# Kernel optimization log

Hardware: AMD Instinct MI355X
Metric: run time of the kernel (lower is better)

The kernel has to match this reference:

```python
import jax, jax.numpy as jnp
import numpy as np

_PRIME = 31
SIZES = tuple(range(3, 21))          # 18 n-gram sizes
TBL = 4096                            # hash table size
MIXED = TBL                           # dedicated mixed/special bucket id
NUM_SIZES_P1 = len(SIZES) + 1         # normalizer (19)
B, L, D = 8, 8192, 256


def _ngram_ids(byte_ids):
    """Rolling polynomial hash ids for every n in SIZES.

    Incremental recurrence: h_k[i] = (h_{k-1}[i-1] * 31 + safe[i]) % TBL
    gives the hash of the backward k-gram ending at i, computing each prefix
    once instead of from scratch per size (same math as the torch loops).
    Returns list of [B, L] int32 id arrays, one per size in SIZES.
    """
    dna_map = jnp.full((14,), -1, dtype=jnp.int32)
    dna_map = dna_map.at[jnp.array([1, 2, 3, 4])].set(jnp.array([0, 1, 2, 3], dtype=jnp.int32))
    dna_idx = dna_map[byte_ids]                      # [B, L], -1 for non-DNA
    safe = jnp.maximum(dna_idx, 0)
    bad1 = dna_idx == -1

    h = safe          # window size k=1 hash
    bad = bad1        # any special token in window / incomplete window
    ids = []
    for k in range(2, max(SIZES) + 1):
        # shift previous-position state right by 1; pad start as bad (incomplete window)
        h = (jnp.pad(h[:, :-1], ((0, 0), (1, 0))) * _PRIME + safe) % TBL
        bad = jnp.pad(bad[:, :-1], ((0, 0), (1, 0)), constant_values=True) | bad1
        if k in SIZES:
            ids.append(jnp.where(bad, MIXED, h))
    return ids


def setup_inputs() -> dict:
    key = jax.random.key(0)
    k1, k2 = jax.random.split(key)
    byte_ids = jax.random.randint(k1, (B, L), 0, 14, dtype=jnp.int32)
    # 18 embedding tables, each [TBL+1, D] (last row = mixed bucket)
    tables = jax.random.normal(k2, (len(SIZES), TBL + 1, D), dtype=jnp.float32) * 0.02
    return {"byte_ids": byte_ids, "tables": tables}


def reference(byte_ids, tables):
    ids = _ngram_ids(byte_ids)
    total = jnp.zeros(byte_ids.shape + (tables.shape[-1],), dtype=tables.dtype)
    for t, id_n in enumerate(ids):
        total = total + tables[t][id_n]            # [B, L, D] gather-accumulate
    return total / NUM_SIZES_P1
```

## Files before the change

### kernel.cpp

```cpp
#include <hip/hip_runtime.h>

#define TBLSZ 4096
#define NSIZES 18
#define DIM 256
#define SEQLEN 8192

__global__ void NGram_smix_kernel(const float* __restrict__ tables,
                                  float* __restrict__ smix) {
    int d = threadIdx.x;
    float s = 0.f;
    for (int t = 0; t < NSIZES; ++t)
        s += tables[((size_t)t * (TBLSZ + 1) + TBLSZ) * DIM + d];
    smix[d] = s;
}

__global__ __launch_bounds__(256) void NGramEmbedding_73718818668652_kernel(
    const int* __restrict__ byte_ids, const float* __restrict__ tables,
    const float* __restrict__ smix, float* __restrict__ out, int npos)
{
    const int tid0   = blockIdx.x * blockDim.x + threadIdx.x;
    const int stride = gridDim.x * blockDim.x;
    const int c = tid0 & 63;
    const float4 base = ((const float4*)smix)[c];
    const float inv = 1.0f / 19.0f;
    const int total = npos * 64;

    for (int tid = tid0; tid < total; tid += stride) {
        const int pos = tid >> 6;
        const int i   = pos & (SEQLEN - 1);
        const int* row = byte_ids + (pos - i);

        float4 acc = base;

        bool slow = false;
        if (i >= 2) {
            int v0 = row[i], v1 = row[i - 1], v2 = row[i - 2];
            slow = ((unsigned)(v0 - 1) < 4u) & ((unsigned)(v1 - 1) < 4u)
                 & ((unsigned)(v2 - 1) < 4u);
        }

        if (slow) {
            int h = 0, p = 1;
            for (int j = 0; j < 20; ++j) {
                const int q = i - j;
                const int v = (q >= 0) ? row[q] : 0;
                if ((unsigned)(v - 1) >= 4u) break;
                h = (h + (v - 1) * p) & (TBLSZ - 1);
                p = (p * 31) & (TBLSZ - 1);
                const int k = j + 1;
                if (k >= 3) {
                    const int t = k - 3;
                    const float4* T4 =
                        (const float4*)(tables + (size_t)t * (TBLSZ + 1) * DIM);
                    float4 g = T4[(size_t)h * (DIM / 4) + c];
                    float4 m = T4[(size_t)TBLSZ * (DIM / 4) + c];
                    acc.x += g.x - m.x; acc.y += g.y - m.y;
                    acc.z += g.z - m.z; acc.w += g.w - m.w;
                }
            }
        }

        float4 r;
        r.x = acc.x * inv; r.y = acc.y * inv;
        r.z = acc.z * inv; r.w = acc.w * inv;
        ((float4*)out)[(size_t)pos * (DIM / 4) + c] = r;
    }
}

extern "C" void kernel_launch(void* const* d_in, const int* in_sizes, int n_in,
                              void* d_out, int out_size, void* d_ws, size_t ws_size,
                              hipStream_t stream) {
    const int*   byte_ids = (const int*)d_in[0];
    const float* tables   = (const float*)d_in[1];
    float* out  = (float*)d_out;
    float* smix = (float*)d_ws;
    const int npos = in_sizes[0];

    hipLaunchKernelGGL(NGram_smix_kernel, dim3(1), dim3(256), 0, stream,
                       tables, smix);
    hipLaunchKernelGGL(NGramEmbedding_73718818668652_kernel,
                       dim3(4096), dim3(256), 0, stream,
                       byte_ids, tables, smix, out, npos);
}
```

Baseline: 24.49 us.

## Split into broadcast fill kernel and sparse ballot-driven correction kernel

The single pass is replaced by a dedicated fill kernel that writes the scaled mixed-bucket sum to every output row, plus a correction kernel. In the correction kernel each lane checks one position and uses a wave ballot to loop only over positions whose last three tokens are DNA, overwriting those rows. The intent is to keep the bulk store loop free of per-position branch checks and to do the hash lookups only where needed. The cost is an extra launch and a second write to the corrected rows.

```diff
diff --git a/kernel.cpp b/kernel.cpp
--- a/kernel.cpp
+++ b/kernel.cpp
@@ -4,66 +4,81 @@
 #define NSIZES 18
 #define DIM 256
 #define SEQLEN 8192
+#define INV19 (1.0f / 19.0f)
 
-__global__ void NGram_smix_kernel(const float* __restrict__ tables,
-                                  float* __restrict__ smix) {
+__global__ void k_smix(const float* __restrict__ tables, float* __restrict__ smix) {
     int d = threadIdx.x;
     float s = 0.f;
+#pragma unroll
     for (int t = 0; t < NSIZES; ++t)
         s += tables[((size_t)t * (TBLSZ + 1) + TBLSZ) * DIM + d];
-    smix[d] = s;
+    smix[d] = s * INV19;
 }
 
-__global__ __launch_bounds__(256) void NGramEmbedding_73718818668652_kernel(
+__global__ __launch_bounds__(256) void k_fill(const float* __restrict__ smix,
+                                              float4* __restrict__ out, int total_f4) {
+    const int t = blockIdx.x * 256 + threadIdx.x;
+    const int stride = gridDim.x * 256;
+    const float4 v = ((const float4*)smix)[t & 63];
+#pragma unroll 4
+    for (int f = t; f < total_f4; f += stride)
+        out[f] = v;
+}
+
+__global__ __launch_bounds__(256) void k_correct(
     const int* __restrict__ byte_ids, const float* __restrict__ tables,
     const float* __restrict__ smix, float* __restrict__ out, int npos)
 {
-    const int tid0   = blockIdx.x * blockDim.x + threadIdx.x;
-    const int stride = gridDim.x * blockDim.x;
-    const int c = tid0 & 63;
-    const float4 base = ((const float4*)smix)[c];
-    const float inv = 1.0f / 19.0f;
-    const int total = npos * 64;
+    const int lane = threadIdx.x & 63;
+    const int posBase = blockIdx.x * 256 + (threadIdx.x >> 6) * 64;
+    const int myPos = posBase + lane;
 
-    for (int tid = tid0; tid < total; tid += stride) {
-        const int pos = tid >> 6;
-        const int i   = pos & (SEQLEN - 1);
-        const int* row = byte_ids + (pos - i);
-
-        float4 acc = base;
-
-        bool slow = false;
+    bool slow = false;
+    if (myPos < npos) {
+        const int i = myPos & (SEQLEN - 1);
         if (i >= 2) {
-            int v0 = row[i], v1 = row[i - 1], v2 = row[i - 2];
+            const int* row = byte_ids + (myPos - i);
+            const int v0 = row[i], v1 = row[i - 1], v2 = row[i - 2];
             slow = ((unsigned)(v0 - 1) < 4u) & ((unsigned)(v1 - 1) < 4u)
                  & ((unsigned)(v2 - 1) < 4u);
         }
+    }
+    unsigned long long mask = __ballot(slow);
+    if (!mask) return;
 
-        if (slow) {
-            int h = 0, p = 1;
-            for (int j = 0; j < 20; ++j) {
-                const int q = i - j;
-                const int v = (q >= 0) ? row[q] : 0;
-                if ((unsigned)(v - 1) >= 4u) break;
-                h = (h + (v - 1) * p) & (TBLSZ - 1);
-                p = (p * 31) & (TBLSZ - 1);
-                const int k = j + 1;
-                if (k >= 3) {
-                    const int t = k - 3;
-                    const float4* T4 =
-                        (const float4*)(tables + (size_t)t * (TBLSZ + 1) * DIM);
-                    float4 g = T4[(size_t)h * (DIM / 4) + c];
-                    float4 m = T4[(size_t)TBLSZ * (DIM / 4) + c];
-                    acc.x += g.x - m.x; acc.y += g.y - m.y;
-                    acc.z += g.z - m.z; acc.w += g.w - m.w;
-                }
+    const float4 basev = ((const float4*)smix)[lane];
+
+    while (mask) {
+        const int b = __ffsll((long long)mask) - 1;
+        mask &= mask - 1;
+        const int pos = posBase + b;
+        const int i = pos & (SEQLEN - 1);
+        const int* row = byte_ids + (pos - i);
+
+        float4 acc = {0.f, 0.f, 0.f, 0.f};
+        int h = 0, p = 1;
+        for (int j = 0; j < 20; ++j) {
+            const int q = i - j;
+            const int v = (q >= 0) ? row[q] : 0;
+            if ((unsigned)(v - 1) >= 4u) break;
+            h = (h + (v - 1) * p) & (TBLSZ - 1);
+            p = (p * 31) & (TBLSZ - 1);
+            const int k = j + 1;
+            if (k >= 3) {
+                const float4* T4 =
+                    (const float4*)(tables + (size_t)(k - 3) * (TBLSZ + 1) * DIM);
+                const float4 g = T4[(size_t)h * (DIM / 4) + lane];
+                const float4 m = T4[(size_t)TBLSZ * (DIM / 4) + lane];
+                acc.x += g.x - m.x; acc.y += g.y - m.y;
+                acc.z += g.z - m.z; acc.w += g.w - m.w;
             }
         }
-
         float4 r;
-        r.x = acc.x * inv; r.y = acc.y * inv;
-        r.z = acc.z * inv; r.w = acc.w * inv;
-        ((float4*)out)[(size_t)pos * (DIM / 4) + c] = r;
+        r.x = basev.x + acc.x * INV19;
+        r.y = basev.y + acc.y * INV19;
+        r.z = basev.z + acc.z * INV19;
+        r.w = basev.w + acc.w * INV19;
+        ((float4*)out)[(size_t)pos * (DIM / 4) + lane] = r;
     }
 }
 
@@ -75,10 +90,11 @@
     float* out  = (float*)d_out;
     float* smix = (float*)d_ws;
     const int npos = in_sizes[0];
+    const int total_f4 = npos * (DIM / 4);
 
-    hipLaunchKernelGGL(NGram_smix_kernel, dim3(1), dim3(256), 0, stream,
-                       tables, smix);
-    hipLaunchKernelGGL(NGramEmbedding_73718818668652_kernel,
-                       dim3(4096), dim3(256), 0, stream,
+    hipLaunchKernelGGL(k_smix, dim3(1), dim3(256), 0, stream, tables, smix);
+    hipLaunchKernelGGL(k_fill, dim3(2048), dim3(256), 0, stream,
+                       smix, (float4*)out, total_f4);
+    hipLaunchKernelGGL(k_correct, dim3((npos + 255) / 256), dim3(256), 0, stream,
                        byte_ids, tables, smix, out, npos);
 }
```

Result: slower. 36.90 us (+50.7%).

## Fuse mixed-row sum into main kernel and ballot-skip windows with no DNA gathers

Applied to the files above, without the earlier changes.

Removes the separate single-block smix kernel and has each wave recompute the 18-table mixed-row sum itself. Work is reorganized so each wave covers 16 positions of a 64-position chunk. A wave-wide ballot over the 3-gram validity check lets slices with no valid n-grams store the constant base row directly. This cuts a kernel launch and per-position branching, at the cost of redundant mixed-row loads per wave and serialized per-position gather loops within a wave.

```diff
diff --git a/kernel.cpp b/kernel.cpp
--- a/kernel.cpp
+++ b/kernel.cpp
@@ -3,67 +3,79 @@
 #define TBLSZ 4096
 #define NSIZES 18
 #define DIM 256
+#define D4 (DIM / 4)
 #define SEQLEN 8192
-
-__global__ void NGram_smix_kernel(const float* __restrict__ tables,
-                                  float* __restrict__ smix) {
-    int d = threadIdx.x;
-    float s = 0.f;
-    for (int t = 0; t < NSIZES; ++t)
-        s += tables[((size_t)t * (TBLSZ + 1) + TBLSZ) * DIM + d];
-    smix[d] = s;
-}
+#define INV19 (1.0f / 19.0f)
+#define CHUNK 64
+#define WPC 4
+#define SLICE (CHUNK / WPC)
 
 __global__ __launch_bounds__(256) void NGramEmbedding_73718818668652_kernel(
     const int* __restrict__ byte_ids, const float* __restrict__ tables,
-    const float* __restrict__ smix, float* __restrict__ out, int npos)
+    float4* __restrict__ out, int nchunk)
 {
-    const int tid0   = blockIdx.x * blockDim.x + threadIdx.x;
-    const int stride = gridDim.x * blockDim.x;
-    const int c = tid0 & 63;
-    const float4 base = ((const float4*)smix)[c];
-    const float inv = 1.0f / 19.0f;
-    const int total = npos * 64;
+    const int lane  = threadIdx.x & 63;
+    const int gwave = (blockIdx.x * 256 + threadIdx.x) >> 6;
+    const int cid   = gwave / WPC;
+    const int sub   = gwave % WPC;
+    if (cid >= nchunk) return;
 
-    for (int tid = tid0; tid < total; tid += stride) {
-        const int pos = tid >> 6;
-        const int i   = pos & (SEQLEN - 1);
-        const int* row = byte_ids + (pos - i);
+    const float4* T4base = (const float4*)tables;
+    float4 base = {0.f, 0.f, 0.f, 0.f};
+#pragma unroll
+    for (int t = 0; t < NSIZES; ++t) {
+        float4 m = T4base[((size_t)t * (TBLSZ + 1) + TBLSZ) * D4 + lane];
+        base.x += m.x; base.y += m.y; base.z += m.z; base.w += m.w;
+    }
+    base.x *= INV19; base.y *= INV19; base.z *= INV19; base.w *= INV19;
 
-        float4 acc = base;
+    const int chunkBase = cid * CHUNK;
+    const int ibase     = chunkBase & (SEQLEN - 1);
+    const int* row      = byte_ids + (chunkBase - ibase);
 
-        bool slow = false;
-        if (i >= 2) {
-            int v0 = row[i], v1 = row[i - 1], v2 = row[i - 2];
-            slow = ((unsigned)(v0 - 1) < 4u) & ((unsigned)(v1 - 1) < 4u)
-                 & ((unsigned)(v2 - 1) < 4u);
+    const int i = ibase + lane;
+    bool slowb = false;
+    if (i >= 2) {
+        const int v0 = row[i], v1 = row[i - 1], v2 = row[i - 2];
+        slowb = ((unsigned)(v0 - 1) < 4u) & ((unsigned)(v1 - 1) < 4u)
+              & ((unsigned)(v2 - 1) < 4u);
+    }
+    const unsigned long long mask = __ballot(slowb);
+
+    const int p0 = sub * SLICE;
+    float4* dst = out + (size_t)(chunkBase + p0) * D4 + lane;
+
+    if (((mask >> p0) & 0xFFFFull) == 0) {
+#pragma unroll
+        for (int p = 0; p < SLICE; ++p)
+            dst[(size_t)p * D4] = base;
+    } else {
+        for (int p = 0; p < SLICE; ++p) {
+            float4 r = base;
+            if ((mask >> (p0 + p)) & 1ull) {
+                const int ii = ibase + p0 + p;
+                float4 acc = {0.f, 0.f, 0.f, 0.f};
+                int h = 0, pw = 1;
+                for (int j = 0; j < 20; ++j) {
+                    const int q = ii - j;
+                    const int v = (q >= 0) ? row[q] : 0;
+                    if ((unsigned)(v - 1) >= 4u) break;
+                    h  = (h + (v - 1) * pw) & (TBLSZ - 1);
+                    pw = (pw * 31) & (TBLSZ - 1);
+                    const int k = j + 1;
+                    if (k >= 3) {
+                        const float4* T4 = T4base + (size_t)(k - 3) * (TBLSZ + 1) * D4;
+                        const float4 g = T4[(size_t)h * D4 + lane];
+                        const float4 m = T4[(size_t)TBLSZ * D4 + lane];
+                        acc.x += g.x - m.x; acc.y += g.y - m.y;
+                        acc.z += g.z - m.z; acc.w += g.w - m.w;
+                    }
+                }
+                r.x += acc.x * INV19; r.y += acc.y * INV19;
+                r.z += acc.z * INV19; r.w += acc.w * INV19;
+            }
+            dst[(size_t)p * D4] = r;
         }
-
-        if (slow) {
-            int h = 0, p = 1;
-            for (int j = 0; j < 20; ++j) {
-                const int q = i - j;
-                const int v = (q >= 0) ? row[q] : 0;
-                if ((unsigned)(v - 1) >= 4u) break;
-                h = (h + (v - 1) * p) & (TBLSZ - 1);
-                p = (p * 31) & (TBLSZ - 1);
-                const int k = j + 1;
-                if (k >= 3) {
-                    const int t = k - 3;
-                    const float4* T4 =
-                        (const float4*)(tables + (size_t)t * (TBLSZ + 1) * DIM);
-                    float4 g = T4[(size_t)h * (DIM / 4) + c];
-                    float4 m = T4[(size_t)TBLSZ * (DIM / 4) + c];
-                    acc.x += g.x - m.x; acc.y += g.y - m.y;
-                    acc.z += g.z - m.z; acc.w += g.w - m.w;
-                }
-            }
-        }
-
-        float4 r;
-        r.x = acc.x * inv; r.y = acc.y * inv;
-        r.z = acc.z * inv; r.w = acc.w * inv;
-        ((float4*)out)[(size_t)pos * (DIM / 4) + c] = r;
     }
 }
 
@@ -72,13 +84,12 @@
                               hipStream_t stream) {
     const int*   byte_ids = (const int*)d_in[0];
     const float* tables   = (const float*)d_in[1];
-    float* out  = (float*)d_out;
-    float* smix = (float*)d_ws;
-    const int npos = in_sizes[0];
+    float* out = (float*)d_out;
+    const int npos   = in_sizes[0];
+    const int nchunk = npos / CHUNK;
+    const int nblocks = (nchunk * WPC * 64) / 256;
 
-    hipLaunchKernelGGL(NGram_smix_kernel, dim3(1), dim3(256), 0, stream,
-                       tables, smix);
     hipLaunchKernelGGL(NGramEmbedding_73718818668652_kernel,
-                       dim3(4096), dim3(256), 0, stream,
-                       byte_ids, tables, smix, out, npos);
+                       dim3(nblocks), dim3(256), 0, stream,
+                       byte_ids, tables, (float4*)out, nchunk);
 }
```

Measured after the change: 24.54 us. Within noise of the previous version (+0.2%).
